# Performance work log

Measured on AMD Instinct MI355X. Metric: run time of the kernel, lower is better.

Reference implementation:

```python
import jax, jax.numpy as jnp
import numpy as np

Q = 400          # num queries
P = 200000       # num points in event
N_INST = 100     # num GT instances
ALPHA = 0.25     # focal alpha
GAMMA = 2.0      # focal gamma
COST_MASK_W = 1.0
COST_DICE_W = 1.0


def setup_inputs() -> dict:
    key = jax.random.key(0)
    k1, k2 = jax.random.split(key)
    pred_masks = jax.random.normal(k1, (Q, P), dtype=jnp.float32)
    labels = jax.random.randint(k2, (P,), 0, N_INST, dtype=jnp.int64 if jax.config.jax_enable_x64 else jnp.int32)
    return {"pred_masks": pred_masks, "labels": labels, "num_instances": N_INST}


def reference(pred_masks, labels, num_instances):
    # pred_masks: [Q, P] mask logits; labels: [P] instance ids in [0, num_instances)
    x = pred_masks.astype(jnp.float32)
    p = jax.nn.sigmoid(x)                      # [Q, P]
    log_p = jax.nn.log_sigmoid(x)              # log sigmoid(x), stable
    log_1mp = jax.nn.log_sigmoid(-x)           # log(1 - sigmoid(x)), stable

    # Focal BCE per point, split by binary target value t in {0,1}:
    #   t=1: alpha     * (1-p)^gamma * (-log p)
    #   t=0: (1-alpha) *    p^gamma  * (-log(1-p))
    f1 = -ALPHA * (1.0 - p) ** GAMMA * log_p        # [Q, P]
    f0 = -(1.0 - ALPHA) * p ** GAMMA * log_1mp      # [Q, P]

    # One-hot GT masks per instance: T[p, j] = 1 iff labels[p] == j
    T = jax.nn.one_hot(labels, num_instances, dtype=jnp.float32)  # [P, N]

    # cost_mask[q, j] = mean_p [ T[p,j]*f1[q,p] + (1-T[p,j])*f0[q,p] ]
    #                 = ( (f1 - f0) @ T + sum_p f0 ) / P   -- avoids [Q,N,P]
    Pn = jnp.asarray(x.shape[1], dtype=jnp.float32)
    cost_mask = (jnp.einsum('qp,pj->qj', f1 - f0, T) + f0.sum(-1, keepdims=True)) / Pn

    # Dice cost (same einsum form as the torch code)
    counts = T.sum(0)                                # [N] points per instance
    numerator = 2.0 * jnp.einsum('qp,pj->qj', p, T)  # [Q, N]
    denominator = p.sum(-1)[:, None] + counts[None, :]
    cost_dice = 1.0 - (numerator + 1.0) / (denominator + 1.0)

    return COST_MASK_W * cost_mask + COST_DICE_W * cost_dice  # [Q, N]
```

## Files before the change

kernel.cpp:

```cpp
#include <hip/hip_runtime.h>
#include <hip/hip_bf16.h>
#include <cstdint>


#define FOCAL_ALPHA 0.25f
constexpr int NMAX   = 128;
constexpr int NTILES = 7;
constexpr int BLOCK  = 256;
constexpr int KC     = 110;

typedef __attribute__((ext_vector_type(8))) short short8;
typedef __attribute__((ext_vector_type(4))) float f32x4;

__device__ __forceinline__ void point_math(float x, float& f1mf0, float& f0o, float& po) {
    float ax  = __builtin_fabsf(x);
    float e   = __expf(-ax);
    float inv = __builtin_amdgcn_rcpf(1.0f + e);
    float p   = (x >= 0.0f) ? inv : e * inv;
    float l   = __logf(1.0f + e);
    float log_p   = fminf(x, 0.0f) - l;
    float log_1mp = fminf(-x, 0.0f) - l;
    float om  = 1.0f - p;
    float f1  = -FOCAL_ALPHA * om * om * log_p;
    float f0  = -(1.0f - FOCAL_ALPHA) * p * p * log_1mp;
    f1mf0 = f1 - f0;
    f0o   = f0;
    po    = p;
}

__device__ __forceinline__ uint32_t pack_bf16_trunc(float lo, float hi) {
    return __builtin_amdgcn_perm(__float_as_uint(hi), __float_as_uint(lo), 0x07060302u);
}

__global__ __launch_bounds__(BLOCK, 3) void
matcher_main(const float* __restrict__ pred, const int* __restrict__ labels,
             float* __restrict__ S1, float* __restrict__ S2,
             float* __restrict__ sumf0, float* __restrict__ sump,
             int Q, int P, int N) {
    const int tid  = threadIdx.x;
    const int wave = tid >> 6;
    const int lane = tid & 63;
    const int m    = lane & 15;
    const int quad = lane >> 4;

    const int strip = blockIdx.y * 4 + wave;
    const int q0    = strip * 16;
    if (q0 >= Q) return;

    const int total_steps = P >> 5;
    const int per         = (total_steps + KC - 1) / KC;
    const int s0          = blockIdx.x * per;
    const int s1          = min(s0 + per, total_steps);
    if (s0 >= s1) return;

    const float* pr = pred + (size_t)(q0 + m) * P + quad * 8 + s0 * 32;
    const int*   lr = labels + quad * 8 + s0 * 32;

    f32x4 c1[NTILES], c2[NTILES];
    #pragma unroll
    for (int t = 0; t < NTILES; ++t) {
        c1[t] = (f32x4){0.f, 0.f, 0.f, 0.f};
        c2[t] = (f32x4){0.f, 0.f, 0.f, 0.f};
    }
    float sf0 = 0.0f, sp = 0.0f;

    union U { uint32_t u[4]; short8 v; };

    float4 cx0 = *(const float4*)pr;
    float4 cx1 = *(const float4*)(pr + 4);
    int4   cl0 = *(const int4*)lr;
    int4   cl1 = *(const int4*)(lr + 4);

    for (int s = s0; s < s1; ++s) {
        pr += 32; lr += 32;
        float4 nx0, nx1; int4 nl0, nl1;
        if (s + 1 < s1) {
            nx0 = *(const float4*)pr;
            nx1 = *(const float4*)(pr + 4);
            nl0 = *(const int4*)lr;
            nl1 = *(const int4*)(lr + 4);
        }

        float xs[8] = {cx0.x, cx0.y, cx0.z, cx0.w, cx1.x, cx1.y, cx1.z, cx1.w};
        int   ls[8] = {cl0.x, cl0.y, cl0.z, cl0.w, cl1.x, cl1.y, cl1.z, cl1.w};

        float v[8], pv[8];
        #pragma unroll
        for (int j = 0; j < 8; ++j) {
            float f0j;
            point_math(xs[j], v[j], f0j, pv[j]);
            sf0 += f0j;
            sp  += pv[j];
        }

        U A1, A2;
        #pragma unroll
        for (int i = 0; i < 4; ++i) {
            A1.u[i] = pack_bf16_trunc(v[2*i],  v[2*i+1]);
            A2.u[i] = pack_bf16_trunc(pv[2*i], pv[2*i+1]);
        }

        #pragma unroll
        for (int t = 0; t < NTILES; ++t) {
            const int tgt = t * 16 + m;
            U B;
            #pragma unroll
            for (int i = 0; i < 4; ++i) {
                uint32_t lo = (ls[2*i]   == tgt) ? 0x00003F80u : 0u;
                uint32_t hi = (ls[2*i+1] == tgt) ? 0x3F800000u : 0u;
                B.u[i] = lo | hi;
            }
            c1[t] = __builtin_amdgcn_mfma_f32_16x16x32_bf16(A1.v, B.v, c1[t], 0, 0, 0);
            c2[t] = __builtin_amdgcn_mfma_f32_16x16x32_bf16(A2.v, B.v, c2[t], 0, 0, 0);
        }

        cx0 = nx0; cx1 = nx1; cl0 = nl0; cl1 = nl1;
    }

    sf0 += __shfl_xor(sf0, 16, 64);
    sf0 += __shfl_xor(sf0, 32, 64);
    sp  += __shfl_xor(sp, 16, 64);
    sp  += __shfl_xor(sp, 32, 64);
    if (lane < 16) {
        unsafeAtomicAdd(&sumf0[q0 + lane], sf0);
        unsafeAtomicAdd(&sump[q0 + lane], sp);
    }

    #pragma unroll
    for (int t = 0; t < NTILES; ++t) {
        const int col = t * 16 + m;
        if (col < N) {
            #pragma unroll
            for (int r = 0; r < 4; ++r) {
                const int row = q0 + quad * 4 + r;
                unsafeAtomicAdd(&S1[(size_t)row * N + col], c1[t][r]);
                unsafeAtomicAdd(&S2[(size_t)row * N + col], c2[t][r]);
            }
        }
    }
}

__global__ __launch_bounds__(256) void
matcher_counts(const int* __restrict__ labels, int* __restrict__ counts, int P, int N) {
    __shared__ int c[NMAX];
    for (int i = threadIdx.x; i < NMAX; i += 256) c[i] = 0;
    __syncthreads();
    const int stride = gridDim.x * 256;
    for (int i = blockIdx.x * 256 + threadIdx.x; i < P; i += stride)
        atomicAdd(&c[labels[i]], 1);
    __syncthreads();
    for (int j = threadIdx.x; j < N; j += 256)
        if (c[j] != 0) atomicAdd(&counts[j], c[j]);
}

__global__ __launch_bounds__(256) void
matcher_final(const float* __restrict__ S1, const float* __restrict__ S2,
              const float* __restrict__ sumf0, const float* __restrict__ sump,
              const int* __restrict__ counts, float* __restrict__ out,
              int Q, int P, int N) {
    int idx = blockIdx.x * 256 + threadIdx.x;
    if (idx >= Q * N) return;
    int q = idx / N;
    int j = idx - q * N;
    float invP = 1.0f / (float)P;
    float cost_mask = (S1[idx] + sumf0[q]) * invP;
    float cost_dice = 1.0f - (2.0f * S2[idx] + 1.0f) / (sump[q] + (float)counts[j] + 1.0f);
    out[idx] = cost_mask + cost_dice;
}

extern "C" void kernel_launch(void* const* d_in, const int* in_sizes, int n_in,
                              void* d_out, int out_size, void* d_ws, size_t ws_size,
                              hipStream_t stream) {
    const float* pred   = (const float*)d_in[0];
    const int*   labels = (const int*)d_in[1];
    const int P = in_sizes[1];
    const int Q = in_sizes[0] / P;
    const int N = out_size / Q;

    float* S1     = (float*)d_ws;
    float* S2     = S1 + (size_t)Q * N;
    float* sumf0  = S2 + (size_t)Q * N;
    float* sump   = sumf0 + Q;
    int*   counts = (int*)(sump + Q);
    size_t ws_used = ((size_t)2 * Q * N + 2 * Q + N) * sizeof(float);

    hipMemsetAsync(d_ws, 0, ws_used, stream);
    matcher_counts<<<64, 256, 0, stream>>>(labels, counts, P, N);

    const int strips = (Q + 15) / 16;
    dim3 grid(KC, (strips + 3) / 4);
    matcher_main<<<grid, BLOCK, 0, stream>>>(pred, labels, S1, S2, sumf0, sump, Q, P, N);

    int qn = Q * N;
    matcher_final<<<(qn + 255) / 256, 256, 0, stream>>>(S1, S2, sumf0, sump, counts,
                                                        (float*)d_out, Q, P, N);
}
```

Measured before the change: 551.4 us.

## Precompute one-hot MFMA B operands in workspace and simplify focal point math

```diff
diff --git a/kernel.cpp b/kernel.cpp
--- a/kernel.cpp
+++ b/kernel.cpp
@@ -12,31 +12,57 @@
 typedef __attribute__((ext_vector_type(8))) short short8;
 typedef __attribute__((ext_vector_type(4))) float f32x4;
 
-__device__ __forceinline__ void point_math(float x, float& f1mf0, float& f0o, float& po) {
-    float ax  = __builtin_fabsf(x);
-    float e   = __expf(-ax);
-    float inv = __builtin_amdgcn_rcpf(1.0f + e);
-    float p   = (x >= 0.0f) ? inv : e * inv;
-    float l   = __logf(1.0f + e);
-    float log_p   = fminf(x, 0.0f) - l;
-    float log_1mp = fminf(-x, 0.0f) - l;
-    float om  = 1.0f - p;
-    float f1  = -FOCAL_ALPHA * om * om * log_p;
-    float f0  = -(1.0f - FOCAL_ALPHA) * p * p * log_1mp;
-    f1mf0 = f1 - f0;
-    f0o   = f0;
-    po    = p;
+__device__ __forceinline__ void point_math(float x, float& d, float& f0o, float& po) {
+    float e  = __expf(-x);
+    float a  = 1.0f + e;
+    float p  = __builtin_amdgcn_rcpf(a);
+    float l  = __logf(a);
+    float lm = -x - l;
+    float om = e * p;
+    float f1 = FOCAL_ALPHA * (om * om) * l;
+    float f0 = -(1.0f - FOCAL_ALPHA) * (p * p) * lm;
+    d   = f1 - f0;
+    f0o = f0;
+    po  = p;
 }
 
 __device__ __forceinline__ uint32_t pack_bf16_trunc(float lo, float hi) {
     return __builtin_amdgcn_perm(__float_as_uint(hi), __float_as_uint(lo), 0x07060302u);
 }
 
-__global__ __launch_bounds__(BLOCK, 3) void
-matcher_main(const float* __restrict__ pred, const int* __restrict__ labels,
-             float* __restrict__ S1, float* __restrict__ S2,
-             float* __restrict__ sumf0, float* __restrict__ sump,
-             int Q, int P, int N) {
+__global__ __launch_bounds__(256) void
+build_B(const int* __restrict__ labels, uint4* __restrict__ Bpre, int steps) {
+    int tid  = blockIdx.x * 256 + threadIdx.x;
+    int step = tid >> 6;
+    int lane = tid & 63;
+    if (step >= steps) return;
+    const int quad = lane >> 4;
+    const int m    = lane & 15;
+    const int base = step * 32 + quad * 8;
+    int4 l0 = *(const int4*)(labels + base);
+    int4 l1 = *(const int4*)(labels + base + 4);
+    int ls[8] = {l0.x, l0.y, l0.z, l0.w, l1.x, l1.y, l1.z, l1.w};
+    #pragma unroll
+    for (int t = 0; t < NTILES; ++t) {
+        const int tgt = t * 16 + m;
+        uint32_t u[4];
+        #pragma unroll
+        for (int i = 0; i < 4; ++i) {
+            uint32_t lo = (ls[2*i]   == tgt) ? 0x00003F80u : 0u;
+            uint32_t hi = (ls[2*i+1] == tgt) ? 0x3F800000u : 0u;
+            u[i] = lo | hi;
+        }
+        Bpre[((size_t)step * NTILES + t) * 64 + lane] = make_uint4(u[0], u[1], u[2], u[3]);
+    }
+}
+
+union BU { uint4 q; short8 v; uint32_t u[4]; };
+
+__global__ __launch_bounds__(BLOCK) void
+matcher_main_pre(const float* __restrict__ pred, const uint4* __restrict__ Bpre,
+                 float* __restrict__ S1, float* __restrict__ S2,
+                 float* __restrict__ sumf0, float* __restrict__ sump,
+                 int Q, int P, int N) {
     const int tid  = threadIdx.x;
     const int wave = tid >> 6;
     const int lane = tid & 63;
@@ -54,7 +80,7 @@
     if (s0 >= s1) return;
 
     const float* pr = pred + (size_t)(q0 + m) * P + quad * 8 + s0 * 32;
-    const int*   lr = labels + quad * 8 + s0 * 32;
+    const uint4* bp = Bpre + (size_t)s0 * (NTILES * 64) + lane;
 
     f32x4 c1[NTILES], c2[NTILES];
     #pragma unroll
@@ -64,7 +90,104 @@
     }
     float sf0 = 0.0f, sp = 0.0f;
 
-    union U { uint32_t u[4]; short8 v; };
+    float4 cx0 = *(const float4*)pr;
+    float4 cx1 = *(const float4*)(pr + 4);
+    BU cb[NTILES];
+    #pragma unroll
+    for (int t = 0; t < NTILES; ++t) cb[t].q = bp[t * 64];
+
+    for (int s = s0; s < s1; ++s) {
+        pr += 32; bp += NTILES * 64;
+        float4 nx0, nx1; BU nb[NTILES];
+        if (s + 1 < s1) {
+            nx0 = *(const float4*)pr;
+            nx1 = *(const float4*)(pr + 4);
+            #pragma unroll
+            for (int t = 0; t < NTILES; ++t) nb[t].q = bp[t * 64];
+        }
+
+        float xs[8] = {cx0.x, cx0.y, cx0.z, cx0.w, cx1.x, cx1.y, cx1.z, cx1.w};
+        float v[8], pv[8];
+        #pragma unroll
+        for (int j = 0; j < 8; ++j) {
+            float f0j;
+            point_math(xs[j], v[j], f0j, pv[j]);
+            sf0 += f0j;
+            sp  += pv[j];
+        }
+
+        BU A1, A2;
+        #pragma unroll
+        for (int i = 0; i < 4; ++i) {
+            A1.u[i] = pack_bf16_trunc(v[2*i],  v[2*i+1]);
+            A2.u[i] = pack_bf16_trunc(pv[2*i], pv[2*i+1]);
+        }
+
+        #pragma unroll
+        for (int t = 0; t < NTILES; ++t) {
+            c1[t] = __builtin_amdgcn_mfma_f32_16x16x32_bf16(A1.v, cb[t].v, c1[t], 0, 0, 0);
+            c2[t] = __builtin_amdgcn_mfma_f32_16x16x32_bf16(A2.v, cb[t].v, c2[t], 0, 0, 0);
+        }
+
+        cx0 = nx0; cx1 = nx1;
+        #pragma unroll
+        for (int t = 0; t < NTILES; ++t) cb[t] = nb[t];
+    }
+
+    sf0 += __shfl_xor(sf0, 16, 64);
+    sf0 += __shfl_xor(sf0, 32, 64);
+    sp  += __shfl_xor(sp, 16, 64);
+    sp  += __shfl_xor(sp, 32, 64);
+    if (lane < 16) {
+        unsafeAtomicAdd(&sumf0[q0 + lane], sf0);
+        unsafeAtomicAdd(&sump[q0 + lane], sp);
+    }
+
+    #pragma unroll
+    for (int t = 0; t < NTILES; ++t) {
+        const int col = t * 16 + m;
+        if (col < N) {
+            #pragma unroll
+            for (int r = 0; r < 4; ++r) {
+                const int row = q0 + quad * 4 + r;
+                unsafeAtomicAdd(&S1[(size_t)row * N + col], c1[t][r]);
+                unsafeAtomicAdd(&S2[(size_t)row * N + col], c2[t][r]);
+            }
+        }
+    }
+}
+
+__global__ __launch_bounds__(BLOCK) void
+matcher_main_fly(const float* __restrict__ pred, const int* __restrict__ labels,
+                 float* __restrict__ S1, float* __restrict__ S2,
+                 float* __restrict__ sumf0, float* __restrict__ sump,
+                 int Q, int P, int N) {
+    const int tid  = threadIdx.x;
+    const int wave = tid >> 6;
+    const int lane = tid & 63;
+    const int m    = lane & 15;
+    const int quad = lane >> 4;
+
+    const int strip = blockIdx.y * 4 + wave;
+    const int q0    = strip * 16;
+    if (q0 >= Q) return;
+
+    const int total_steps = P >> 5;
+    const int per         = (total_steps + KC - 1) / KC;
+    const int s0          = blockIdx.x * per;
+    const int s1          = min(s0 + per, total_steps);
+    if (s0 >= s1) return;
+
+    const float* pr = pred + (size_t)(q0 + m) * P + quad * 8 + s0 * 32;
+    const int*   lr = labels + quad * 8 + s0 * 32;
+
+    f32x4 c1[NTILES], c2[NTILES];
+    #pragma unroll
+    for (int t = 0; t < NTILES; ++t) {
+        c1[t] = (f32x4){0.f, 0.f, 0.f, 0.f};
+        c2[t] = (f32x4){0.f, 0.f, 0.f, 0.f};
+    }
+    float sf0 = 0.0f, sp = 0.0f;
 
     float4 cx0 = *(const float4*)pr;
     float4 cx1 = *(const float4*)(pr + 4);
@@ -83,7 +206,6 @@
 
         float xs[8] = {cx0.x, cx0.y, cx0.z, cx0.w, cx1.x, cx1.y, cx1.z, cx1.w};
         int   ls[8] = {cl0.x, cl0.y, cl0.z, cl0.w, cl1.x, cl1.y, cl1.z, cl1.w};
-
         float v[8], pv[8];
         #pragma unroll
         for (int j = 0; j < 8; ++j) {
@@ -93,7 +215,7 @@
             sp  += pv[j];
         }
 
-        U A1, A2;
+        BU A1, A2;
         #pragma unroll
         for (int i = 0; i < 4; ++i) {
             A1.u[i] = pack_bf16_trunc(v[2*i],  v[2*i+1]);
@@ -103,7 +225,7 @@
         #pragma unroll
         for (int t = 0; t < NTILES; ++t) {
             const int tgt = t * 16 + m;
-            U B;
+            BU B;
             #pragma unroll
             for (int i = 0; i < 4; ++i) {
                 uint32_t lo = (ls[2*i]   == tgt) ? 0x00003F80u : 0u;
@@ -182,14 +304,26 @@
     float* sumf0  = S2 + (size_t)Q * N;
     float* sump   = sumf0 + Q;
     int*   counts = (int*)(sump + Q);
-    size_t ws_used = ((size_t)2 * Q * N + 2 * Q + N) * sizeof(float);
-
-    hipMemsetAsync(d_ws, 0, ws_used, stream);
+    size_t base_bytes = ((size_t)2 * Q * N + 2 * Q + N) * sizeof(float);
+
+    const int steps = P >> 5;
+    size_t bpre_off   = (base_bytes + 255) & ~(size_t)255;
+    size_t bpre_bytes = (size_t)steps * NTILES * 64 * sizeof(uint4);
+    bool use_pre = (ws_size >= bpre_off + bpre_bytes);
+
+    hipMemsetAsync(d_ws, 0, base_bytes, stream);
     matcher_counts<<<64, 256, 0, stream>>>(labels, counts, P, N);
 
     const int strips = (Q + 15) / 16;
     dim3 grid(KC, (strips + 3) / 4);
-    matcher_main<<<grid, BLOCK, 0, stream>>>(pred, labels, S1, S2, sumf0, sump, Q, P, N);
+
+    if (use_pre) {
+        uint4* Bpre = (uint4*)((char*)d_ws + bpre_off);
+        build_B<<<(steps * 64 + 255) / 256, 256, 0, stream>>>(labels, Bpre, steps);
+        matcher_main_pre<<<grid, BLOCK, 0, stream>>>(pred, Bpre, S1, S2, sumf0, sump, Q, P, N);
+    } else {
+        matcher_main_fly<<<grid, BLOCK, 0, stream>>>(pred, labels, S1, S2, sumf0, sump, Q, P, N);
+    }
 
     int qn = Q * N;
     matcher_final<<<(qn + 255) / 256, 256, 0, stream>>>(S1, S2, sumf0, sump, counts,
```

Result: no change. 550.3 us (-0.2%).
